# Kernel optimization log

Hardware: AMD Instinct MI355X
Metric: run time of the kernel (lower is better)

The kernel has to match this reference:

```python
import jax, jax.numpy as jnp
import numpy as np

H = 256          # LSTM hidden per direction
C = 512          # input / BN channels
TEMP_SCALE = 10.0
GUMBEL_TEMP = 0.8
BN_EPS = 1e-5
GUM_EPS = 1e-20
K = 5            # median pool kernel


def _lstm_dir(xs, Wih, Whh, bih, bhh, reverse):
    # xs: [T, B, C]; gate order i, f, g, o (PyTorch convention)
    T, B, _ = xs.shape
    proj = jnp.einsum('tbc,gc->tbg', xs, Wih) + bih + bhh  # [T, B, 4H]
    h0 = jnp.zeros((B, H), xs.dtype)

    def step(carry, p):
        h, c = carry
        g = p + h @ Whh.T
        i, f, gg, o = jnp.split(g, 4, axis=-1)
        i = jax.nn.sigmoid(i); f = jax.nn.sigmoid(f)
        gg = jnp.tanh(gg); o = jax.nn.sigmoid(o)
        c = f * c + i * gg
        h = o * jnp.tanh(c)
        return (h, c), h

    _, hs = jax.lax.scan(step, (h0, h0), proj, reverse=reverse)
    return hs  # [T, B, H], time-aligned


def _median_pool(x):
    # x: [B, 1, T], kernel 5, stride 1, 'same' via reflect pad
    T = x.shape[-1]
    xp = jnp.pad(x, ((0, 0), (0, 0), (2, 2)), mode='reflect')
    w = jnp.stack([xp[:, :, i:i + T] for i in range(K)], axis=-1)  # [B,1,T,5]
    return jnp.sort(w, axis=-1)[..., K // 2]


def _forward(x, e, u, Wih_f, Whh_f, bih_f, bhh_f, Wih_b, Whh_b, bih_b, bhh_b,
             gamma, beta, Wlin, blin):
    # x: [B, C, T] -> [T, B, C]
    xs = jnp.transpose(x, (2, 0, 1))
    hf = _lstm_dir(xs, Wih_f, Whh_f, bih_f, bhh_f, reverse=False)
    hb = _lstm_dir(xs, Wih_b, Whh_b, bih_b, bhh_b, reverse=True)
    h = jnp.concatenate([hf, hb], axis=-1)          # [T, B, 2H]

    # BatchNorm1d (training mode: batch stats over B and T), channels = 2H
    hb_ = jnp.transpose(h, (1, 2, 0))               # [B, 2H, T]
    mean = jnp.mean(hb_, axis=(0, 2), keepdims=True)
    var = jnp.mean((hb_ - mean) ** 2, axis=(0, 2), keepdims=True)
    hn = (hb_ - mean) * jax.lax.rsqrt(var + BN_EPS)
    hn = hn * gamma[None, :, None] + beta[None, :, None]

    # Linear(512 -> 2) then tempered softmax
    z = jnp.einsum('bct,oc->bto', hn, Wlin) + blin   # [B, T, 2]
    posterior = jax.nn.softmax(z / TEMP_SCALE, axis=-1)

    # Gumbel-softmax straight-through on log(posterior)
    g = -jnp.log(-jnp.log(u + GUM_EPS) + GUM_EPS)
    y = jax.nn.softmax((jnp.log(posterior) + g) / GUMBEL_TEMP, axis=-1)
    ind = jnp.argmax(y, axis=-1)
    y_hard = jax.nn.one_hot(ind, 2, dtype=y.dtype)
    st = jax.lax.stop_gradient(y_hard - y) + y       # [B, T, 2]

    sampled = jnp.transpose(st[:, :, 1:2], (0, 2, 1)) * e[:, :, :st.shape[1]]  # [B,1,T]
    mask = _median_pool(sampled)
    mask = _median_pool(_median_pool(mask))
    return posterior, mask


def setup_inputs() -> dict:
    key = jax.random.key(0)
    ks = jax.random.split(key, 16)
    B, T = 16, 2048
    s = 0.05
    return {
        'x': jax.random.normal(ks[0], (B, C, T), jnp.float32),
        'e': jax.random.uniform(ks[1], (B, 1, T), jnp.float32),
        'u': jax.random.uniform(ks[2], (B, T, 2), jnp.float32,
                                minval=1e-6, maxval=1.0 - 1e-6),
        'Wih_f': jax.random.normal(ks[3], (4 * H, C), jnp.float32) * s,
        'Whh_f': jax.random.normal(ks[4], (4 * H, H), jnp.float32) * s,
        'bih_f': jax.random.normal(ks[5], (4 * H,), jnp.float32) * s,
        'bhh_f': jax.random.normal(ks[6], (4 * H,), jnp.float32) * s,
        'Wih_b': jax.random.normal(ks[7], (4 * H, C), jnp.float32) * s,
        'Whh_b': jax.random.normal(ks[8], (4 * H, H), jnp.float32) * s,
        'bih_b': jax.random.normal(ks[9], (4 * H,), jnp.float32) * s,
        'bhh_b': jax.random.normal(ks[10], (4 * H,), jnp.float32) * s,
        'gamma': jnp.ones((2 * H,), jnp.float32),
        'beta': jnp.zeros((2 * H,), jnp.float32),
        'Wlin': jax.random.normal(ks[11], (2, 2 * H), jnp.float32) * s,
        'blin': jnp.zeros((2,), jnp.float32),
    }


def reference(x, e, u, Wih_f, Whh_f, bih_f, bhh_f, Wih_b, Whh_b, bih_b, bhh_b,
              gamma, beta, Wlin, blin):
    return _forward(x, e, u, Wih_f, Whh_f, bih_f, bhh_f, Wih_b, Whh_b,
                    bih_b, bhh_b, gamma, beta, Wlin, blin)
```

## Files before the change

### kernel.cpp

```cpp
#include <hip/hip_runtime.h>
#include <math.h>

#define H    256
#define G4H  1024
#define CIN  512
#define BB   16
#define TT   2048
#define CHUNK 128
#define NPH  16

typedef unsigned long long ull;

#define OFF_WQ      ((size_t)0)
#define OFF_PF0     ((size_t)524288)
#define OFF_PF1     ((size_t)2621440)
#define OFF_PB0     ((size_t)4718592)
#define OFF_PB1     ((size_t)6815744)
#define OFF_HBUF    ((size_t)8912896)
#define OFF_STATS   ((size_t)25690112)
#define OFF_CSTATE  ((size_t)25691136)
#define OFF_HX      ((size_t)25699328)
#define OFF_W2      ((size_t)25732096)
#define OFF_B2      ((size_t)25733120)
#define OFF_SAMP    ((size_t)25733136)
#define OFF_HLAST   ((size_t)25765904)

#define REP16(X) X(0) X(1) X(2) X(3) X(4) X(5) X(6) X(7) X(8) X(9) X(10) X(11) \
  X(12) X(13) X(14) X(15)

__device__ __forceinline__ float frcp_(float x) { return __builtin_amdgcn_rcpf(x); }
__device__ __forceinline__ float fsig_(float x) { return frcp_(1.f + __expf(-x)); }
__device__ __forceinline__ float ftanh_(float x) {
  float a = fabsf(x);
  float e = __expf(-2.f * a);
  float t = (1.f - e) * frcp_(1.f + e);
  return copysignf(t, x);
}

__global__ __launch_bounds__(256) void k0_init(
    const float* __restrict__ WhhF, const float* __restrict__ WhhB,
    float4* __restrict__ wq, float* __restrict__ stats, int* __restrict__ hxw) {
  int idx = blockIdx.x * 256 + threadIdx.x;
  if (idx < 131072) {
    int jl = idx & 31, s = (idx >> 5) & 7, gate = (idx >> 8) & 3;
    int q = (idx >> 10) & 15, kq = (idx >> 14) & 3, dir = idx >> 16;
    int row = gate * 256 + s * 32 + jl;
    int col = kq * 64 + q * 4;
    const float* W = (dir ? WhhB : WhhF) + (size_t)row * H + col;
    wq[idx] = make_float4(W[0], W[1], W[2], W[3]);
  }
  if (idx < 1024) stats[idx] = 0.f;
  if (idx < 32768) hxw[idx] = 0;
}

__global__ __launch_bounds__(512, 1) void k12(
    const float4* __restrict__ wq,
    const float* __restrict__ pF2, const float* __restrict__ pB2,
    float* __restrict__ pF1, float* __restrict__ pB1,
    const float* __restrict__ x,
    const float* __restrict__ WihF, const float* __restrict__ bihF, const float* __restrict__ bhhF,
    const float* __restrict__ WihB, const float* __restrict__ bihB, const float* __restrict__ bhhB,
    float* __restrict__ hbuf, ull* __restrict__ hx2, float* __restrict__ hlast,
    float* __restrict__ cstate, float* __restrict__ stats,
    int nk2, int t0f2, int t0b2, int first, int ebase, int p1) {
  __shared__ __align__(16) float smem[16 * 68 + 16 * 132];

  if ((int)blockIdx.x < nk2) {
    float* h_lds = smem;
    float* pbuf  = smem + 256;
    const int tid = threadIdx.x;
    const int l = tid & 63, w = tid >> 6;
    const int jl = tid & 31, gate = (tid >> 5) & 3, kq = tid >> 7;
    const int bx = blockIdx.x;
    const int grp = bx & 31, s = bx >> 5;
    const int dir = grp >> 4, b = grp & 15;
    const int row = gate * 256 + s * 32 + jl;

    const float4* wbase = wq + (size_t)(dir * 4 + kq) * 16384 + gate * 256 + s * 32 + jl;
#define WDECL(i) float wx##i, wy##i, wz##i, ww##i; \
    { float4 t_ = wbase[(size_t)(i) * 1024]; \
      wx##i = t_.x; wy##i = t_.y; wz##i = t_.z; ww##i = t_.w; } \
    asm volatile("" : "+v"(wx##i), "+v"(wy##i), "+v"(wz##i), "+v"(ww##i));
    REP16(WDECL)
#undef WDECL

    float c = 0.f, s1 = 0.f, s2 = 0.f;
    if (w == 0 && l < 32 && !first) c = cstate[grp * 256 + s * 32 + l];

    const float* pbase = dir ? pB2 : pF2;
    float pv = 0.f;
    if (kq == 0) {
      int tc0 = dir ? (CHUNK - 1) : 0;
      pv = pbase[((size_t)tc0 * BB + b) * G4H + row];
    }

    for (int step = 0; step < CHUNK; ++step) {
      int abs = ebase + step;

      if (tid < 256) {
        if (abs == 0) {
          h_lds[tid] = 0.f;
        } else if (step == 0) {
          h_lds[tid] = hlast[grp * 256 + tid];
        } else if ((tid >> 5) != s) {
          ull* src = hx2 + (size_t)((abs - 1) & 1) * 8192 + grp * 256 + tid;
          ull wd = __hip_atomic_load(src, __ATOMIC_RELAXED, __HIP_MEMORY_SCOPE_AGENT);
          while ((int)(wd >> 32) < abs)
            wd = __hip_atomic_load(src, __ATOMIC_RELAXED, __HIP_MEMORY_SCOPE_AGENT);
          h_lds[tid] = __uint_as_float((unsigned)wd);
        }
      }
      __syncthreads();

      float acc = (kq == 0) ? pv : 0.f;
      const float4* h4p = ((const float4*)h_lds) + (kq << 4);
#define WFMA(i) { float4 hv = h4p[i]; \
      acc += wx##i * hv.x + wy##i * hv.y + wz##i * hv.z + ww##i * hv.w; }
      REP16(WFMA)
#undef WFMA
      pbuf[tid] = acc;
      __syncthreads();

      if (w == 0 && l < 32) {
        float gi = pbuf[l]       + pbuf[128 + l] + pbuf[256 + l] + pbuf[384 + l];
        float gf = pbuf[32 + l]  + pbuf[160 + l] + pbuf[288 + l] + pbuf[416 + l];
        float gg = pbuf[64 + l]  + pbuf[192 + l] + pbuf[320 + l] + pbuf[448 + l];
        float go = pbuf[96 + l]  + pbuf[224 + l] + pbuf[352 + l] + pbuf[480 + l];
        float ig = fsig_(gi);
        float fg = fsig_(gf);
        float gz = ftanh_(gg);
        float og = fsig_(go);
        c = fg * c + ig * gz;
        float h = og * ftanh_(c);
        s1 += h; s2 += h * h;
        int j = s * 32 + l;
        h_lds[j] = h;
        ull wd = ((ull)(unsigned)(abs + 1) << 32) | (ull)__float_as_uint(h);
        __hip_atomic_store(hx2 + (size_t)(abs & 1) * 8192 + grp * 256 + j, wd,
                           __ATOMIC_RELAXED, __HIP_MEMORY_SCOPE_AGENT);
        if (step == CHUNK - 1) hlast[grp * 256 + j] = h;
        int tc = dir ? (CHUNK - 1 - step) : step;
        int t = (dir ? t0b2 : t0f2) + tc;
        hbuf[((size_t)t * BB + b) * 512 + dir * 256 + j] = h;
      }
      if (kq == 0 && step + 1 < CHUNK) {
        int tcn = dir ? (CHUNK - 2 - step) : (step + 1);
        pv = pbase[((size_t)tcn * BB + b) * G4H + row];
      }
    }

    if (w == 0 && l < 32) {
      cstate[grp * 256 + s * 32 + l] = c;
      atomicAdd(&stats[dir * 256 + s * 32 + l], s1);
      atomicAdd(&stats[512 + dir * 256 + s * 32 + l], s2);
    }
    return;
  }

  if (p1 < 0) return;
  float* Xs = smem;
  float* Ws = smem + 16 * 68;
  int bid = (int)blockIdx.x - nk2;
  int ttile = bid & 1, gtile = (bid >> 1) & 7, zb = bid >> 4;
  int b = zb & 15, dir = zb >> 4;
  const float* Wih = dir ? WihB : WihF;
  const float* bih = dir ? bihB : bihF;
  const float* bhh = dir ? bhhB : bhhF;
  float* proj = dir ? pB1 : pF1;
  int t0 = (dir ? (NPH - 1 - p1) : p1) * CHUNK;
  int tbase = t0 + ttile * 64;
  int gbase = gtile * 128;
  int tid = threadIdx.x;
  int tx = tid & 15, ty = tid >> 4;
  float acc[4][4];
#pragma unroll
  for (int i = 0; i < 4; i++)
#pragma unroll
    for (int j = 0; j < 4; j++) acc[i][j] = 0.f;

  int lt = tid & 63, lk = tid >> 6;
  int wg = tid >> 2, wc = tid & 3;
  const float* xb = x + (size_t)b * CIN * TT + tbase + lt;
  const float* wp = Wih + (size_t)(gbase + wg) * CIN + 4 * wc;

  float rxa = xb[(size_t)lk * TT];
  float rxb = xb[(size_t)(lk + 8) * TT];
  float4 rw = *(const float4*)wp;

  for (int c0 = 0; c0 < CIN; c0 += 16) {
    __syncthreads();
    Xs[lk * 68 + lt] = rxa;
    Xs[(lk + 8) * 68 + lt] = rxb;
    Ws[(4 * wc + 0) * 132 + wg] = rw.x;
    Ws[(4 * wc + 1) * 132 + wg] = rw.y;
    Ws[(4 * wc + 2) * 132 + wg] = rw.z;
    Ws[(4 * wc + 3) * 132 + wg] = rw.w;
    __syncthreads();
    if (c0 + 16 < CIN) {
      rxa = xb[(size_t)(c0 + 16 + lk) * TT];
      rxb = xb[(size_t)(c0 + 16 + lk + 8) * TT];
      rw  = *(const float4*)(wp + c0 + 16);
    }
#pragma unroll
    for (int kk = 0; kk < 16; kk++) {
      float4 av = *(const float4*)&Xs[kk * 68 + tx * 4];
      float4 bv = *(const float4*)&Ws[kk * 132 + ty * 4];
      acc[0][0] += av.x * bv.x; acc[0][1] += av.x * bv.y; acc[0][2] += av.x * bv.z; acc[0][3] += av.x * bv.w;
      acc[1][0] += av.y * bv.x; acc[1][1] += av.y * bv.y; acc[1][2] += av.y * bv.z; acc[1][3] += av.y * bv.w;
      acc[2][0] += av.z * bv.x; acc[2][1] += av.z * bv.y; acc[2][2] += av.z * bv.z; acc[2][3] += av.z * bv.w;
      acc[3][0] += av.w * bv.x; acc[3][1] += av.w * bv.y; acc[3][2] += av.w * bv.z; acc[3][3] += av.w * bv.w;
    }
  }
  int g0 = gbase + ty * 4;
  float bias0 = bih[g0 + 0] + bhh[g0 + 0];
  float bias1 = bih[g0 + 1] + bhh[g0 + 1];
  float bias2 = bih[g0 + 2] + bhh[g0 + 2];
  float bias3 = bih[g0 + 3] + bhh[g0 + 3];
#pragma unroll
  for (int i = 0; i < 4; i++) {
    int tc = ttile * 64 + tx * 4 + i;
    float4 st = make_float4(acc[i][0] + bias0, acc[i][1] + bias1,
                            acc[i][2] + bias2, acc[i][3] + bias3);
    *(float4*)(proj + ((size_t)tc * BB + b) * G4H + g0) = st;
  }
}

__global__ __launch_bounds__(512) void k3_prep(
    const float* __restrict__ stats, const float* __restrict__ gamma,
    const float* __restrict__ beta, const float* __restrict__ Wlin,
    const float* __restrict__ blin, float* __restrict__ w2, float* __restrict__ b2) {
  __shared__ float r0[512], r1[512];
  int ch = threadIdx.x;
  float mean = stats[ch] * (1.f / 32768.f);
  float var  = stats[512 + ch] * (1.f / 32768.f) - mean * mean;
  float sc = gamma[ch] * rsqrtf(var + 1e-5f);
  float w0 = Wlin[ch], w1 = Wlin[512 + ch];
  w2[ch] = w0 * sc; w2[512 + ch] = w1 * sc;
  float tt = beta[ch] - mean * sc;
  r0[ch] = w0 * tt; r1[ch] = w1 * tt;
  __syncthreads();
  for (int off = 256; off > 0; off >>= 1) {
    if (ch < off) { r0[ch] += r0[ch + off]; r1[ch] += r1[ch + off]; }
    __syncthreads();
  }
  if (ch == 0) { b2[0] = blin[0] + r0[0]; b2[1] = blin[1] + r1[0]; }
}

__global__ __launch_bounds__(256) void k4_post(
    const float* __restrict__ hbuf, const float* __restrict__ w2,
    const float* __restrict__ b2, const float* __restrict__ u,
    const float* __restrict__ e, float* __restrict__ post,
    float* __restrict__ samp) {
  int wid = (blockIdx.x * 256 + threadIdx.x) >> 6;
  int lane = threadIdx.x & 63;
  int b = wid >> 11, t = wid & 2047;
  const float* hr = hbuf + ((size_t)t * BB + b) * 512;
  int c0 = lane * 8;
  float4 h0 = *(const float4*)(hr + c0);
  float4 h1 = *(const float4*)(hr + c0 + 4);
  float4 wa = *(const float4*)(w2 + c0);
  float4 wb = *(const float4*)(w2 + c0 + 4);
  float4 va = *(const float4*)(w2 + 512 + c0);
  float4 vb = *(const float4*)(w2 + 512 + c0 + 4);
  float d0 = h0.x * wa.x + h0.y * wa.y + h0.z * wa.z + h0.w * wa.w
           + h1.x * wb.x + h1.y * wb.y + h1.z * wb.z + h1.w * wb.w;
  float d1 = h0.x * va.x + h0.y * va.y + h0.z * va.z + h0.w * va.w
           + h1.x * vb.x + h1.y * vb.y + h1.z * vb.z + h1.w * vb.w;
#pragma unroll
  for (int off = 32; off > 0; off >>= 1) {
    d0 += __shfl_xor(d0, off, 64);
    d1 += __shfl_xor(d1, off, 64);
  }
  if (lane == 0) {
    float z0 = (d0 + b2[0]) * 0.1f, z1 = (d1 + b2[1]) * 0.1f;
    float m = fmaxf(z0, z1);
    float e0 = expf(z0 - m), e1 = expf(z1 - m);
    float inv = 1.f / (e0 + e1);
    float p0 = e0 * inv, p1 = e1 * inv;
    size_t o = (size_t)b * TT + t;
    post[o * 2] = p0; post[o * 2 + 1] = p1;
    float u0 = u[o * 2], u1 = u[o * 2 + 1];
    float g0 = -logf(-logf(u0 + 1e-20f) + 1e-20f);
    float g1 = -logf(-logf(u1 + 1e-20f) + 1e-20f);
    float a0 = logf(p0) + g0, a1 = logf(p1) + g1;
    samp[o] = (a1 > a0) ? e[o] : 0.f;
  }
}

#define MSWAP(a, b) { float lo_ = fminf(a, b); b = fmaxf(a, b); a = lo_; }
__global__ __launch_bounds__(256) void k5_median(
    const float* __restrict__ samp, float* __restrict__ mask) {
  __shared__ float buf[2][TT];
  int b = blockIdx.x, tid = threadIdx.x;
  for (int i = tid; i < TT; i += 256) buf[0][i] = samp[(size_t)b * TT + i];
  __syncthreads();
  int src = 0;
  for (int pass = 0; pass < 3; ++pass) {
    for (int i = tid; i < TT; i += 256) {
      float v0, v1, v2, v3, v4;
      {
        int i0 = i - 2; i0 = i0 < 0 ? -i0 : i0;
        int i1 = i - 1; i1 = i1 < 0 ? -i1 : i1;
        int i3 = i + 1; i3 = i3 > TT - 1 ? 2 * (TT - 1) - i3 : i3;
        int i4 = i + 2; i4 = i4 > TT - 1 ? 2 * (TT - 1) - i4 : i4;
        v0 = buf[src][i0]; v1 = buf[src][i1]; v2 = buf[src][i];
        v3 = buf[src][i3]; v4 = buf[src][i4];
      }
      MSWAP(v0, v1); MSWAP(v3, v4); MSWAP(v2, v4); MSWAP(v2, v3);
      MSWAP(v1, v4); MSWAP(v0, v3); MSWAP(v0, v2); MSWAP(v1, v3);
      MSWAP(v1, v2);
      buf[1 - src][i] = v2;
    }
    __syncthreads();
    src = 1 - src;
  }
  for (int i = tid; i < TT; i += 256) mask[(size_t)b * TT + i] = buf[src][i];
}

extern "C" void kernel_launch(void* const* d_in, const int* in_sizes, int n_in,
                              void* d_out, int out_size, void* d_ws, size_t ws_size,
                              hipStream_t stream) {
  const float* x    = (const float*)d_in[0];
  const float* e    = (const float*)d_in[1];
  const float* u    = (const float*)d_in[2];
  const float* WihF = (const float*)d_in[3];
  const float* WhhF = (const float*)d_in[4];
  const float* bihF = (const float*)d_in[5];
  const float* bhhF = (const float*)d_in[6];
  const float* WihB = (const float*)d_in[7];
  const float* WhhB = (const float*)d_in[8];
  const float* bihB = (const float*)d_in[9];
  const float* bhhB = (const float*)d_in[10];
  const float* gamma= (const float*)d_in[11];
  const float* beta = (const float*)d_in[12];
  const float* Wlin = (const float*)d_in[13];
  const float* blin = (const float*)d_in[14];

  float* ws = (float*)d_ws;
  float4* wq    = (float4*)(ws + OFF_WQ);
  float* pf[2]  = { ws + OFF_PF0, ws + OFF_PF1 };
  float* pb[2]  = { ws + OFF_PB0, ws + OFF_PB1 };
  float* hbuf   = ws + OFF_HBUF;
  float* stats  = ws + OFF_STATS;
  float* cstate = ws + OFF_CSTATE;
  ull*   hx2    = (ull*)(ws + OFF_HX);
  float* w2     = ws + OFF_W2;
  float* b2     = ws + OFF_B2;
  float* samp   = ws + OFF_SAMP;
  float* hlast  = ws + OFF_HLAST;

  float* post = (float*)d_out;
  float* mask = (float*)d_out + (size_t)BB * TT * 2;

  hipLaunchKernelGGL(k0_init, dim3(512), dim3(256), 0, stream,
                     WhhF, WhhB, wq, stats, (int*)hx2);
  hipLaunchKernelGGL(k12, dim3(512), dim3(512), 0, stream,
                     wq, pf[0], pb[0], pf[0], pb[0], x,
                     WihF, bihF, bhhF, WihB, bihB, bhhB,
                     hbuf, hx2, hlast, cstate, stats,
                     0, 0, 0, 1, 0, 0);
  for (int p = 0; p < NPH; ++p) {
    int q = p & 1;
    int np1 = (p + 1 < NPH) ? (p + 1) : -1;
    int nblk = 256 + ((np1 >= 0) ? 512 : 0);
    hipLaunchKernelGGL(k12, dim3(nblk), dim3(512), 0, stream,
                       wq, pf[q], pb[q], pf[q ^ 1], pb[q ^ 1], x,
                       WihF, bihF, bhhF, WihB, bihB, bhhB,
                       hbuf, hx2, hlast, cstate, stats,
                       256, p * CHUNK, (NPH - 1 - p) * CHUNK,
                       p == 0 ? 1 : 0, p * CHUNK, np1);
  }
  hipLaunchKernelGGL(k3_prep, dim3(1), dim3(512), 0, stream,
                     stats, gamma, beta, Wlin, blin, w2, b2);
  hipLaunchKernelGGL(k4_post, dim3(8192), dim3(256), 0, stream,
                     hbuf, w2, b2, u, e, post, samp);
  hipLaunchKernelGGL(k5_median, dim3(16), dim3(256), 0, stream, samp, mask);
}
```

Baseline: 3.082 ms.

## Process forward and backward LSTM directions in one block to halve recurrent blocks

Each recurrent block now handles one batch element for both directions, keeping both directions' Whh slices in registers (128 floats per thread instead of 64). The two directions are stepped alternately within each time step, and the recurrent block count drops from 256 to 128. The aim is to free CUs for the overlapped projection GEMM and to reduce the number of spinning blocks. The cost is serialized work per step, roughly twice the per-block latency on the critical recurrence path, plus higher register pressure.

```diff
diff --git a/kernel.cpp b/kernel.cpp
--- a/kernel.cpp
+++ b/kernel.cpp
@@ -66,32 +66,42 @@
   __shared__ __align__(16) float smem[16 * 68 + 16 * 132];
 
   if ((int)blockIdx.x < nk2) {
-    float* h_lds = smem;
-    float* pbuf  = smem + 256;
+    float* h_ldsA = smem;
+    float* h_ldsB = smem + 256;
+    float* pbuf   = smem + 512;
     const int tid = threadIdx.x;
     const int l = tid & 63, w = tid >> 6;
     const int jl = tid & 31, gate = (tid >> 5) & 3, kq = tid >> 7;
     const int bx = blockIdx.x;
-    const int grp = bx & 31, s = bx >> 5;
-    const int dir = grp >> 4, b = grp & 15;
+    const int b = bx & 15, s = bx >> 4;
+    const int gA = b, gB = 16 + b;
     const int row = gate * 256 + s * 32 + jl;
 
-    const float4* wbase = wq + (size_t)(dir * 4 + kq) * 16384 + gate * 256 + s * 32 + jl;
-#define WDECL(i) float wx##i, wy##i, wz##i, ww##i; \
-    { float4 t_ = wbase[(size_t)(i) * 1024]; \
-      wx##i = t_.x; wy##i = t_.y; wz##i = t_.z; ww##i = t_.w; } \
-    asm volatile("" : "+v"(wx##i), "+v"(wy##i), "+v"(wz##i), "+v"(ww##i));
-    REP16(WDECL)
-#undef WDECL
-
-    float c = 0.f, s1 = 0.f, s2 = 0.f;
-    if (w == 0 && l < 32 && !first) c = cstate[grp * 256 + s * 32 + l];
-
-    const float* pbase = dir ? pB2 : pF2;
-    float pv = 0.f;
+    const float4* wbA = wq + (size_t)(kq) * 16384 + gate * 256 + s * 32 + jl;
+    const float4* wbB = wq + (size_t)(4 + kq) * 16384 + gate * 256 + s * 32 + jl;
+#define WDECLA(i) float ax##i, ay##i, az##i, aw##i; \
+    { float4 t_ = wbA[(size_t)(i) * 1024]; \
+      ax##i = t_.x; ay##i = t_.y; az##i = t_.z; aw##i = t_.w; } \
+    asm volatile("" : "+v"(ax##i), "+v"(ay##i), "+v"(az##i), "+v"(aw##i));
+    REP16(WDECLA)
+#undef WDECLA
+#define WDECLB(i) float bx##i, by##i, bz##i, bw##i; \
+    { float4 t_ = wbB[(size_t)(i) * 1024]; \
+      bx##i = t_.x; by##i = t_.y; bz##i = t_.z; bw##i = t_.w; } \
+    asm volatile("" : "+v"(bx##i), "+v"(by##i), "+v"(bz##i), "+v"(bw##i));
+    REP16(WDECLB)
+#undef WDECLB
+
+    float cA = 0.f, cB = 0.f, s1A = 0.f, s2A = 0.f, s1B = 0.f, s2B = 0.f;
+    if (w == 0 && l < 32 && !first) {
+      cA = cstate[gA * 256 + s * 32 + l];
+      cB = cstate[gB * 256 + s * 32 + l];
+    }
+
+    float pvA = 0.f, pvB = 0.f;
     if (kq == 0) {
-      int tc0 = dir ? (CHUNK - 1) : 0;
-      pv = pbase[((size_t)tc0 * BB + b) * G4H + row];
+      pvA = pF2[((size_t)0 * BB + b) * G4H + row];
+      pvB = pB2[((size_t)(CHUNK - 1) * BB + b) * G4H + row];
     }
 
     for (int step = 0; step < CHUNK; ++step) {
@@ -99,25 +109,27 @@
 
       if (tid < 256) {
         if (abs == 0) {
-          h_lds[tid] = 0.f;
+          h_ldsA[tid] = 0.f;
         } else if (step == 0) {
-          h_lds[tid] = hlast[grp * 256 + tid];
+          h_ldsA[tid] = hlast[gA * 256 + tid];
         } else if ((tid >> 5) != s) {
-          ull* src = hx2 + (size_t)((abs - 1) & 1) * 8192 + grp * 256 + tid;
+          ull* src = hx2 + (size_t)((abs - 1) & 1) * 8192 + gA * 256 + tid;
           ull wd = __hip_atomic_load(src, __ATOMIC_RELAXED, __HIP_MEMORY_SCOPE_AGENT);
           while ((int)(wd >> 32) < abs)
             wd = __hip_atomic_load(src, __ATOMIC_RELAXED, __HIP_MEMORY_SCOPE_AGENT);
-          h_lds[tid] = __uint_as_float((unsigned)wd);
+          h_ldsA[tid] = __uint_as_float((unsigned)wd);
         }
       }
       __syncthreads();
 
-      float acc = (kq == 0) ? pv : 0.f;
-      const float4* h4p = ((const float4*)h_lds) + (kq << 4);
+      float acc = (kq == 0) ? pvA : 0.f;
+      {
+        const float4* h4p = ((const float4*)h_ldsA) + (kq << 4);
 #define WFMA(i) { float4 hv = h4p[i]; \
-      acc += wx##i * hv.x + wy##i * hv.y + wz##i * hv.z + ww##i * hv.w; }
-      REP16(WFMA)
+        acc += ax##i * hv.x + ay##i * hv.y + az##i * hv.z + aw##i * hv.w; }
+        REP16(WFMA)
 #undef WFMA
+      }
       pbuf[tid] = acc;
       __syncthreads();
 
@@ -126,33 +138,77 @@
         float gf = pbuf[32 + l]  + pbuf[160 + l] + pbuf[288 + l] + pbuf[416 + l];
         float gg = pbuf[64 + l]  + pbuf[192 + l] + pbuf[320 + l] + pbuf[448 + l];
         float go = pbuf[96 + l]  + pbuf[224 + l] + pbuf[352 + l] + pbuf[480 + l];
-        float ig = fsig_(gi);
-        float fg = fsig_(gf);
-        float gz = ftanh_(gg);
-        float og = fsig_(go);
-        c = fg * c + ig * gz;
-        float h = og * ftanh_(c);
-        s1 += h; s2 += h * h;
+        float ig = fsig_(gi), fg = fsig_(gf), gz = ftanh_(gg), og = fsig_(go);
+        cA = fg * cA + ig * gz;
+        float h = og * ftanh_(cA);
+        s1A += h; s2A += h * h;
         int j = s * 32 + l;
-        h_lds[j] = h;
+        h_ldsA[j] = h;
         ull wd = ((ull)(unsigned)(abs + 1) << 32) | (ull)__float_as_uint(h);
-        __hip_atomic_store(hx2 + (size_t)(abs & 1) * 8192 + grp * 256 + j, wd,
+        __hip_atomic_store(hx2 + (size_t)(abs & 1) * 8192 + gA * 256 + j, wd,
                            __ATOMIC_RELAXED, __HIP_MEMORY_SCOPE_AGENT);
-        if (step == CHUNK - 1) hlast[grp * 256 + j] = h;
-        int tc = dir ? (CHUNK - 1 - step) : step;
-        int t = (dir ? t0b2 : t0f2) + tc;
-        hbuf[((size_t)t * BB + b) * 512 + dir * 256 + j] = h;
-      }
-      if (kq == 0 && step + 1 < CHUNK) {
-        int tcn = dir ? (CHUNK - 2 - step) : (step + 1);
-        pv = pbase[((size_t)tcn * BB + b) * G4H + row];
-      }
+        if (step == CHUNK - 1) hlast[gA * 256 + j] = h;
+        int t = t0f2 + step;
+        hbuf[((size_t)t * BB + b) * 512 + j] = h;
+      }
+      if (kq == 0 && step + 1 < CHUNK)
+        pvA = pF2[((size_t)(step + 1) * BB + b) * G4H + row];
+
+      if (tid < 256) {
+        if (abs == 0) {
+          h_ldsB[tid] = 0.f;
+        } else if (step == 0) {
+          h_ldsB[tid] = hlast[gB * 256 + tid];
+        } else if ((tid >> 5) != s) {
+          ull* src = hx2 + (size_t)((abs - 1) & 1) * 8192 + gB * 256 + tid;
+          ull wd = __hip_atomic_load(src, __ATOMIC_RELAXED, __HIP_MEMORY_SCOPE_AGENT);
+          while ((int)(wd >> 32) < abs)
+            wd = __hip_atomic_load(src, __ATOMIC_RELAXED, __HIP_MEMORY_SCOPE_AGENT);
+          h_ldsB[tid] = __uint_as_float((unsigned)wd);
+        }
+      }
+      __syncthreads();
+
+      acc = (kq == 0) ? pvB : 0.f;
+      {
+        const float4* h4p = ((const float4*)h_ldsB) + (kq << 4);
+#define WFMA(i) { float4 hv = h4p[i]; \
+        acc += bx##i * hv.x + by##i * hv.y + bz##i * hv.z + bw##i * hv.w; }
+        REP16(WFMA)
+#undef WFMA
+      }
+      pbuf[tid] = acc;
+      __syncthreads();
+
+      if (w == 0 && l < 32) {
+        float gi = pbuf[l]       + pbuf[128 + l] + pbuf[256 + l] + pbuf[384 + l];
+        float gf = pbuf[32 + l]  + pbuf[160 + l] + pbuf[288 + l] + pbuf[416 + l];
+        float gg = pbuf[64 + l]  + pbuf[192 + l] + pbuf[320 + l] + pbuf[448 + l];
+        float go = pbuf[96 + l]  + pbuf[224 + l] + pbuf[352 + l] + pbuf[480 + l];
+        float ig = fsig_(gi), fg = fsig_(gf), gz = ftanh_(gg), og = fsig_(go);
+        cB = fg * cB + ig * gz;
+        float h = og * ftanh_(cB);
+        s1B += h; s2B += h * h;
+        int j = s * 32 + l;
+        h_ldsB[j] = h;
+        ull wd = ((ull)(unsigned)(abs + 1) << 32) | (ull)__float_as_uint(h);
+        __hip_atomic_store(hx2 + (size_t)(abs & 1) * 8192 + gB * 256 + j, wd,
+                           __ATOMIC_RELAXED, __HIP_MEMORY_SCOPE_AGENT);
+        if (step == CHUNK - 1) hlast[gB * 256 + j] = h;
+        int t = t0b2 + (CHUNK - 1 - step);
+        hbuf[((size_t)t * BB + b) * 512 + 256 + j] = h;
+      }
+      if (kq == 0 && step + 1 < CHUNK)
+        pvB = pB2[((size_t)(CHUNK - 2 - step) * BB + b) * G4H + row];
     }
 
     if (w == 0 && l < 32) {
-      cstate[grp * 256 + s * 32 + l] = c;
-      atomicAdd(&stats[dir * 256 + s * 32 + l], s1);
-      atomicAdd(&stats[512 + dir * 256 + s * 32 + l], s2);
+      cstate[gA * 256 + s * 32 + l] = cA;
+      cstate[gB * 256 + s * 32 + l] = cB;
+      atomicAdd(&stats[s * 32 + l], s1A);
+      atomicAdd(&stats[512 + s * 32 + l], s2A);
+      atomicAdd(&stats[256 + s * 32 + l], s1B);
+      atomicAdd(&stats[768 + s * 32 + l], s2B);
     }
     return;
   }
@@ -362,12 +418,12 @@
   for (int p = 0; p < NPH; ++p) {
     int q = p & 1;
     int np1 = (p + 1 < NPH) ? (p + 1) : -1;
-    int nblk = 256 + ((np1 >= 0) ? 512 : 0);
+    int nblk = 128 + ((np1 >= 0) ? 512 : 0);
     hipLaunchKernelGGL(k12, dim3(nblk), dim3(512), 0, stream,
                        wq, pf[q], pb[q], pf[q ^ 1], pb[q ^ 1], x,
                        WihF, bihF, bhhF, WihB, bihB, bhhB,
                        hbuf, hx2, hlast, cstate, stats,
-                       256, p * CHUNK, (NPH - 1 - p) * CHUNK,
+                       128, p * CHUNK, (NPH - 1 - p) * CHUNK,
                        p == 0 ? 1 : 0, p * CHUNK, np1);
   }
   hipLaunchKernelGGL(k3_prep, dim3(1), dim3(512), 0, stream,
```

Result: slower. 4.585 ms (+48.7%).
